# Performance work log

Hardware: AMD Instinct MI355X
Metric: run time of the kernel (lower is better)

The kernel has to match this reference:

```python
import jax, jax.numpy as jnp
import numpy as np

V = 25000
E = 100000
NODE_IN = 74
EDGE_IN = 12
OUT = 64
EHID = 128
NUM_STEPS = 6


def setup_inputs() -> dict:
    key = jax.random.key(0)
    ks = jax.random.split(key, 12)
    s = 0.05
    node_feats = jax.random.normal(ks[0], (V, NODE_IN), dtype=jnp.float32)
    edge_feats = jax.random.normal(ks[1], (E, EDGE_IN), dtype=jnp.float32)
    src = jax.random.randint(ks[2], (E,), 0, V)
    dst = jax.random.randint(ks[3], (E,), 0, V)
    # project_node_feats: Linear(node_in, out)
    Wp = jax.random.normal(ks[4], (NODE_IN, OUT), dtype=jnp.float32) * s
    bp = jnp.zeros((OUT,), dtype=jnp.float32)
    # edge network: Linear(edge_in, ehid) -> ReLU -> Linear(ehid, out*out)
    We1 = jax.random.normal(ks[5], (EDGE_IN, EHID), dtype=jnp.float32) * s
    be1 = jnp.zeros((EHID,), dtype=jnp.float32)
    We2 = jax.random.normal(ks[6], (EHID, OUT * OUT), dtype=jnp.float32) * s
    be2 = jnp.zeros((OUT * OUT,), dtype=jnp.float32)
    # NNConv output bias
    bias = jnp.zeros((OUT,), dtype=jnp.float32)
    return {
        "node_feats": node_feats, "edge_feats": edge_feats,
        "src": src, "dst": dst,
        "Wp": Wp, "bp": bp,
        "We1": We1, "be1": be1, "We2": We2, "be2": be2,
        "bias": bias,
    }


def reference(node_feats, edge_feats, src, dst, Wp, bp, We1, be1, We2, be2, bias):
    # project node features
    h = jax.nn.relu(node_feats @ Wp + bp)  # [V, OUT]
    # per-edge weight matrices (same every step -> hoist out of loop)
    ew = jax.nn.relu(edge_feats @ We1 + be1) @ We2 + be2  # [E, OUT*OUT]
    ew = ew.reshape(E, OUT, OUT)
    for _ in range(NUM_STEPS):
        # gather src node feats, batched matvec, scatter-sum to dst
        msg = jnp.einsum('ei,eio->eo', h[src], ew)  # [E, OUT]
        agg = jax.ops.segment_sum(msg, dst, num_segments=V)  # [V, OUT]
        h = jax.nn.relu(agg + bias)
    return h
```

## Files before the change

kernel.cpp:

```cpp
#include <hip/hip_runtime.h>
#include <hip/hip_bf16.h>

#define Vn 25000
#define En 100000
#define NODE_IN 74
#define EDGE_IN 12
#define OUTD 64
#define EHID 128
#define NUM_STEPS 6

#define HPAD 68

typedef __attribute__((ext_vector_type(8))) _Float16 half8;
typedef __attribute__((ext_vector_type(4))) float floatx4;

__global__ void proj_kernel(const float* __restrict__ node,
                            const float* __restrict__ Wp,
                            const float* __restrict__ bp,
                            float* __restrict__ h) {
  __shared__ float nf[NODE_IN];
  int v = blockIdx.x;
  int o = threadIdx.x;
  for (int i = o; i < NODE_IN; i += 64) nf[i] = node[(size_t)v * NODE_IN + i];
  __syncthreads();
  float acc = bp[o];
  for (int i = 0; i < NODE_IN; ++i) acc = fmaf(nf[i], Wp[i * OUTD + o], acc);
  h[(size_t)v * OUTD + o] = fmaxf(acc, 0.0f);
}

__global__ void edge_kernel(const float* __restrict__ ef,
                            const float* __restrict__ We1,
                            const float* __restrict__ be1,
                            _Float16* __restrict__ f) {
  __shared__ float es[EDGE_IN];
  int e = blockIdx.x;
  int k = threadIdx.x;
  if (k < EDGE_IN) es[k] = ef[(size_t)e * EDGE_IN + k];
  __syncthreads();
  float acc = be1[k];
  for (int j = 0; j < EDGE_IN; ++j) acc = fmaf(es[j], We1[j * EHID + k], acc);
  f[(size_t)e * EHID + k] = (_Float16)fmaxf(acc, 0.0f);
}

__global__ void w2r_kernel(const float* __restrict__ We2,
                           _Float16* __restrict__ w2s) {
  int g = blockIdx.x * 256 + threadIdx.x;
  int j = g & 7;
  int quad = (g >> 3) & 3;
  int l15 = (g >> 5) & 15;
  int s = (g >> 9) & 3;
  int wv = (g >> 11) & 3;
  int i = g >> 13;
  int k = s * 32 + quad * 8 + j;
  int col = i * 64 + wv * 16 + l15;
  w2s[g] = (_Float16)We2[(size_t)k * (OUTD * OUTD) + col];
}

__global__ __launch_bounds__(256) void msg_kernel(
    const float* __restrict__ h,
    const _Float16* __restrict__ f,
    const _Float16* __restrict__ w2s,
    const int* __restrict__ src,
    const int* __restrict__ dst,
    const float* __restrict__ be2,
    float* __restrict__ agg) {
  __shared__ float h_t[64 * HPAD];
  __shared__ int s_dst[64];

  const int tid = threadIdx.x;
  const int wv = tid >> 6;
  const int lane = tid & 63;
  const int quad = lane >> 4;
  const int l15 = lane & 15;
  const int e0 = blockIdx.x * 64;

  if (tid < 64) {
    int e = e0 + tid;
    s_dst[tid] = (e < En) ? dst[e] : -1;
  }
  {
    int e = tid & 63;
    int ib = tid >> 6;
    int eg = e0 + e;
    int sv = (eg < En) ? src[eg] : 0;
    const float4* hp = reinterpret_cast<const float4*>(h + (size_t)sv * OUTD + ib * 16);
    for (int c = 0; c < 4; ++c) {
      float4 val = hp[c];
      int i4 = ib * 16 + c * 4;
      h_t[(i4 + 0) * HPAD + e] = val.x;
      h_t[(i4 + 1) * HPAD + e] = val.y;
      h_t[(i4 + 2) * HPAD + e] = val.z;
      h_t[(i4 + 3) * HPAD + e] = val.w;
    }
  }
  __syncthreads();

  half8 afr[4][4];
  for (int t = 0; t < 4; ++t) {
    int e = e0 + t * 16 + l15;
    if (e >= En) e = En - 1;
    const _Float16* fr = f + (size_t)e * EHID + quad * 8;
    for (int s = 0; s < 4; ++s)
      afr[t][s] = *reinterpret_cast<const half8*>(fr + s * 32);
  }

  const _Float16* w2b = w2s + wv * 2048 + l15 * 32 + quad * 8;

#define LOADB(dstv, ii)                                                     \
  {                                                                         \
    const _Float16* p_ = w2b + (size_t)(ii) * 8192;                         \
    dstv[0] = *reinterpret_cast<const half8*>(p_);                          \
    dstv[1] = *reinterpret_cast<const half8*>(p_ + 512);                    \
    dstv[2] = *reinterpret_cast<const half8*>(p_ + 1024);                   \
    dstv[3] = *reinterpret_cast<const half8*>(p_ + 1536);                   \
  }

  floatx4 msgacc[4];
  const floatx4 zero4 = (floatx4){0.f, 0.f, 0.f, 0.f};
  for (int t = 0; t < 4; ++t) msgacc[t] = zero4;

  half8 ba[4], bb[4];
  LOADB(ba, 0);
  LOADB(bb, 1);

#define BODY(iv, breg)                                                         \
  {                                                                            \
    _Float16 hf[4];                                                            \
    for (int t = 0; t < 4; ++t)                                                \
      hf[t] = (_Float16)h_t[(iv) * HPAD + t * 16 + l15];                       \
    half8 hb[4];                                                               \
    for (int t = 0; t < 4; ++t)                                                \
      hb[t] = (half8){hf[t], hf[t], hf[t], hf[t], hf[t], hf[t], hf[t], hf[t]}; \
    for (int s = 0; s < 4; ++s)                                                \
      for (int t = 0; t < 4; ++t) {                                            \
        half8 as = afr[t][s] * hb[t];                                          \
        msgacc[t] = __builtin_amdgcn_mfma_f32_16x16x32_f16(as, breg[s],        \
                                                           msgacc[t], 0, 0, 0); \
      }                                                                        \
  }

  for (int ii = 0; ii < 32; ++ii) {
    int i0 = 2 * ii;
    BODY(i0, ba);
    {
      int inx = (i0 + 2 < 64) ? i0 + 2 : 63;
      LOADB(ba, inx);
    }
    BODY(i0 + 1, bb);
    {
      int inx = (i0 + 3 < 64) ? i0 + 3 : 63;
      LOADB(bb, inx);
    }
  }

  {
    half8 b2f8[2];
    for (int s = 0; s < 2; ++s) {
      half8 v;
      for (int j = 0; j < 8; ++j)
        v[j] = (_Float16)be2[(s * 32 + quad * 8 + j) * 64 + wv * 16 + l15];
      b2f8[s] = v;
    }
    for (int t = 0; t < 4; ++t) {
      half8 ha[2];
      for (int s = 0; s < 2; ++s)
        for (int j = 0; j < 8; ++j)
          ha[s][j] = (_Float16)h_t[(s * 32 + quad * 8 + j) * HPAD + t * 16 + l15];
      msgacc[t] = __builtin_amdgcn_mfma_f32_16x16x32_f16(ha[0], b2f8[0], msgacc[t], 0, 0, 0);
      msgacc[t] = __builtin_amdgcn_mfma_f32_16x16x32_f16(ha[1], b2f8[1], msgacc[t], 0, 0, 0);
    }
  }

  int col = wv * 16 + l15;
  for (int t = 0; t < 4; ++t) {
    int rb = t * 16 + quad * 4;
    for (int r = 0; r < 4; ++r) {
      int d = s_dst[rb + r];
      if (d >= 0) atomicAdd(&agg[(size_t)d * OUTD + col], msgacc[t][r]);
    }
  }
}

__global__ void update_kernel(float* __restrict__ agg,
                              const float* __restrict__ bias,
                              float* __restrict__ hout,
                              float* __restrict__ dout, int last) {
  int g = blockIdx.x * 256 + threadIdx.x;
  if (g >= Vn * OUTD) return;
  float v = agg[g];
  agg[g] = 0.0f;
  float r = fmaxf(v + bias[g & 63], 0.0f);
  hout[g] = r;
  if (last) dout[g] = r;
}

extern "C" void kernel_launch(void* const* d_in, const int* in_sizes, int n_in,
                              void* d_out, int out_size, void* d_ws, size_t ws_size,
                              hipStream_t stream) {
  const float* node = (const float*)d_in[0];
  const float* edge = (const float*)d_in[1];
  const int* src = (const int*)d_in[2];
  const int* dst = (const int*)d_in[3];
  const float* Wp   = (const float*)d_in[4];
  const float* bp   = (const float*)d_in[5];
  const float* We1  = (const float*)d_in[6];
  const float* be1  = (const float*)d_in[7];
  const float* We2  = (const float*)d_in[8];
  const float* be2  = (const float*)d_in[9];
  const float* bias = (const float*)d_in[10];
  float* out = (float*)d_out;

  char* ws = (char*)d_ws;
  float* agg = (float*)(ws);
  float* h_a = (float*)(ws + 6400000);
  float* h_b = (float*)(ws + 12800000);
  _Float16* f   = (_Float16*)(ws + 19200000);
  _Float16* w2s = (_Float16*)(ws + 44800000);

  hipMemsetAsync(agg, 0, (size_t)Vn * OUTD * sizeof(float), stream);
  proj_kernel<<<Vn, 64, 0, stream>>>(node, Wp, bp, h_a);
  edge_kernel<<<En, 128, 0, stream>>>(edge, We1, be1, f);
  w2r_kernel<<<(OUTD * OUTD * EHID) / 256, 256, 0, stream>>>(We2, w2s);

  float* hin = h_a;
  float* hout = h_b;
  for (int s = 0; s < NUM_STEPS; ++s) {
    msg_kernel<<<(En + 63) / 64, 256, 0, stream>>>(hin, f, w2s, src, dst, be2, agg);
    update_kernel<<<(Vn * OUTD + 255) / 256, 256, 0, stream>>>(
        agg, bias, hout, out, s == NUM_STEPS - 1);
    float* t = hin; hin = hout; hout = t;
  }
}
```

Before: 925.4 us.

## Switch message kernel to 32x32x16 MFMA tiles with 2x2 wave layout

Replaces the 16x16x32 MFMA tiling, where each wave covered 64 edges by 16 output columns, with 32x32x16 MFMA. Each wave now covers 32 edges by 32 output columns in a 2x2 split across the four waves, and the W2 shuffle layout is rewritten to match. The edge-hidden fragments per wave drop from 16 to 8 half8 registers, and the per-step h broadcast shrinks to one value. Each wave now loads twice as many B fragments per i-step, 8 half8 instead of 4, while the A-fragment loads per wave are halved. The total MFMA FLOPs stay the same.

```diff
diff --git a/kernel.cpp b/kernel.cpp
--- a/kernel.cpp
+++ b/kernel.cpp
@@ -12,7 +12,7 @@
 #define HPAD 68
 
 typedef __attribute__((ext_vector_type(8))) _Float16 half8;
-typedef __attribute__((ext_vector_type(4))) float floatx4;
+typedef __attribute__((ext_vector_type(16))) float floatx16;
 
 __global__ void proj_kernel(const float* __restrict__ node,
                             const float* __restrict__ Wp,
@@ -46,13 +46,12 @@
                            _Float16* __restrict__ w2s) {
   int g = blockIdx.x * 256 + threadIdx.x;
   int j = g & 7;
-  int quad = (g >> 3) & 3;
-  int l15 = (g >> 5) & 15;
-  int s = (g >> 9) & 3;
-  int wv = (g >> 11) & 3;
+  int lane = (g >> 3) & 63;
+  int s = (g >> 9) & 7;
+  int c = (g >> 12) & 1;
   int i = g >> 13;
-  int k = s * 32 + quad * 8 + j;
-  int col = i * 64 + wv * 16 + l15;
+  int k = s * 16 + 8 * (lane >> 5) + j;
+  int col = i * 64 + c * 32 + (lane & 31);
   w2s[g] = (_Float16)We2[(size_t)k * (OUTD * OUTD) + col];
 }
 
@@ -68,10 +67,12 @@
   __shared__ int s_dst[64];
 
   const int tid = threadIdx.x;
-  const int wv = tid >> 6;
+  const int wvq = tid >> 6;
+  const int eh = wvq >> 1;
+  const int ch = wvq & 1;
   const int lane = tid & 63;
-  const int quad = lane >> 4;
-  const int l15 = lane & 15;
+  const int l31 = lane & 31;
+  const int lh = lane >> 5;
   const int e0 = blockIdx.x * 64;
 
   if (tid < 64) {
@@ -84,9 +85,9 @@
     int eg = e0 + e;
     int sv = (eg < En) ? src[eg] : 0;
     const float4* hp = reinterpret_cast<const float4*>(h + (size_t)sv * OUTD + ib * 16);
-    for (int c = 0; c < 4; ++c) {
-      float4 val = hp[c];
-      int i4 = ib * 16 + c * 4;
+    for (int cc = 0; cc < 4; ++cc) {
+      float4 val = hp[cc];
+      int i4 = ib * 16 + cc * 4;
       h_t[(i4 + 0) * HPAD + e] = val.x;
       h_t[(i4 + 1) * HPAD + e] = val.y;
       h_t[(i4 + 2) * HPAD + e] = val.z;
@@ -95,16 +96,16 @@
   }
   __syncthreads();
 
-  half8 afr[4][4];
-  for (int t = 0; t < 4; ++t) {
-    int e = e0 + t * 16 + l15;
+  half8 afr[8];
+  {
+    int e = e0 + eh * 32 + l31;
     if (e >= En) e = En - 1;
-    const _Float16* fr = f + (size_t)e * EHID + quad * 8;
-    for (int s = 0; s < 4; ++s)
-      afr[t][s] = *reinterpret_cast<const half8*>(fr + s * 32);
-  }
-
-  const _Float16* w2b = w2s + wv * 2048 + l15 * 32 + quad * 8;
+    const _Float16* fr = f + (size_t)e * EHID + 8 * lh;
+    for (int s = 0; s < 8; ++s)
+      afr[s] = *reinterpret_cast<const half8*>(fr + s * 16);
+  }
+
+  const _Float16* w2b = w2s + ch * 4096 + lane * 8;
 
 #define LOADB(dstv, ii)                                                     \
   {                                                                         \
@@ -113,30 +114,26 @@
     dstv[1] = *reinterpret_cast<const half8*>(p_ + 512);                    \
     dstv[2] = *reinterpret_cast<const half8*>(p_ + 1024);                   \
     dstv[3] = *reinterpret_cast<const half8*>(p_ + 1536);                   \
-  }
-
-  floatx4 msgacc[4];
-  const floatx4 zero4 = (floatx4){0.f, 0.f, 0.f, 0.f};
-  for (int t = 0; t < 4; ++t) msgacc[t] = zero4;
-
-  half8 ba[4], bb[4];
+    dstv[4] = *reinterpret_cast<const half8*>(p_ + 2048);                   \
+    dstv[5] = *reinterpret_cast<const half8*>(p_ + 2560);                   \
+    dstv[6] = *reinterpret_cast<const half8*>(p_ + 3072);                   \
+    dstv[7] = *reinterpret_cast<const half8*>(p_ + 3584);                   \
+  }
+
+  floatx16 acc = (floatx16){0.f};
+
+  half8 ba[8], bb[8];
   LOADB(ba, 0);
   LOADB(bb, 1);
 
-#define BODY(iv, breg)                                                         \
-  {                                                                            \
-    _Float16 hf[4];                                                            \
-    for (int t = 0; t < 4; ++t)                                                \
-      hf[t] = (_Float16)h_t[(iv) * HPAD + t * 16 + l15];                       \
-    half8 hb[4];                                                               \
-    for (int t = 0; t < 4; ++t)                                                \
-      hb[t] = (half8){hf[t], hf[t], hf[t], hf[t], hf[t], hf[t], hf[t], hf[t]}; \
-    for (int s = 0; s < 4; ++s)                                                \
-      for (int t = 0; t < 4; ++t) {                                            \
-        half8 as = afr[t][s] * hb[t];                                          \
-        msgacc[t] = __builtin_amdgcn_mfma_f32_16x16x32_f16(as, breg[s],        \
-                                                           msgacc[t], 0, 0, 0); \
-      }                                                                        \
+#define BODY(iv, breg)                                                        \
+  {                                                                           \
+    _Float16 hh = (_Float16)h_t[(iv) * HPAD + eh * 32 + l31];                 \
+    half8 hb = (half8){hh, hh, hh, hh, hh, hh, hh, hh};                       \
+    for (int s = 0; s < 8; ++s) {                                             \
+      half8 as = afr[s] * hb;                                                 \
+      acc = __builtin_amdgcn_mfma_f32_32x32x16_f16(as, breg[s], acc, 0, 0, 0); \
+    }                                                                         \
   }
 
   for (int ii = 0; ii < 32; ++ii) {
@@ -154,30 +151,22 @@
   }
 
   {
-    half8 b2f8[2];
-    for (int s = 0; s < 2; ++s) {
-      half8 v;
-      for (int j = 0; j < 8; ++j)
-        v[j] = (_Float16)be2[(s * 32 + quad * 8 + j) * 64 + wv * 16 + l15];
-      b2f8[s] = v;
-    }
-    for (int t = 0; t < 4; ++t) {
-      half8 ha[2];
-      for (int s = 0; s < 2; ++s)
-        for (int j = 0; j < 8; ++j)
-          ha[s][j] = (_Float16)h_t[(s * 32 + quad * 8 + j) * HPAD + t * 16 + l15];
-      msgacc[t] = __builtin_amdgcn_mfma_f32_16x16x32_f16(ha[0], b2f8[0], msgacc[t], 0, 0, 0);
-      msgacc[t] = __builtin_amdgcn_mfma_f32_16x16x32_f16(ha[1], b2f8[1], msgacc[t], 0, 0, 0);
-    }
-  }
-
-  int col = wv * 16 + l15;
-  for (int t = 0; t < 4; ++t) {
-    int rb = t * 16 + quad * 4;
-    for (int r = 0; r < 4; ++r) {
-      int d = s_dst[rb + r];
-      if (d >= 0) atomicAdd(&agg[(size_t)d * OUTD + col], msgacc[t][r]);
-    }
+    for (int s = 0; s < 4; ++s) {
+      half8 ha, b2;
+      for (int j = 0; j < 8; ++j) {
+        int i = s * 16 + 8 * lh + j;
+        ha[j] = (_Float16)h_t[i * HPAD + eh * 32 + l31];
+        b2[j] = (_Float16)be2[i * 64 + ch * 32 + l31];
+      }
+      acc = __builtin_amdgcn_mfma_f32_32x32x16_f16(ha, b2, acc, 0, 0, 0);
+    }
+  }
+
+  int col = ch * 32 + l31;
+  for (int reg = 0; reg < 16; ++reg) {
+    int r = (reg & 3) + 8 * (reg >> 2) + 4 * lh;
+    int d = s_dst[eh * 32 + r];
+    if (d >= 0) atomicAdd(&agg[(size_t)d * OUTD + col], acc[reg]);
   }
 }
 
```

Result: slower. 990.4 us (+7.0%).
